# Performance work log

Hardware: AMD Instinct MI355X
Metric: run time of the kernel (lower is better)

## Reference

```python
import jax, jax.numpy as jnp
import numpy as np
from jax import lax

NMS_THRESH = 0.7
PRE_NMS_TOPK = 1000
POST_NMS_TOPK = 256
MIN_SIZE = 0.0


def setup_inputs() -> dict:
    key = jax.random.key(0)
    ks = jax.random.split(key, 4)
    N, C, Hf, Wf, P = 2, 128, 256, 256, 9
    x = jax.random.normal(ks[0], (N, C, Hf, Wf), jnp.float32)
    # small weight scales keep exp(offsets*stride) in a sane range (offsets head is zero-init in torch)
    W_conv = jax.random.normal(ks[1], (C, C, 3, 3), jnp.float32) * 0.05
    b_conv = jnp.zeros((C,), jnp.float32)
    W_off = jax.random.normal(ks[2], (2 * P, C), jnp.float32) * 0.01
    b_off = jnp.zeros((2 * P,), jnp.float32)
    W_log = jax.random.normal(ks[3], (1, C), jnp.float32) * 0.05
    b_log = jnp.zeros((1,), jnp.float32)
    return {"x": x, "W_conv": W_conv, "b_conv": b_conv, "W_off": W_off,
            "b_off": b_off, "W_log": W_log, "b_log": b_log,
            "image_h": 2048, "image_w": 2048}


def _forward_dense(x, W_conv, b_conv, W_off, b_off, W_log, b_log, image_h, image_w):
    N, C, Hf, Wf = x.shape
    t = lax.conv_general_dilated(x, W_conv, (1, 1), ((1, 1), (1, 1)),
                                 dimension_numbers=("NCHW", "OIHW", "NCHW"))
    t = jax.nn.relu(t + b_conv[None, :, None, None])
    logits = jnp.einsum("nchw,oc->nohw", t, W_log) + b_log[None, :, None, None]  # (N,1,Hf,Wf)
    off = jnp.einsum("nchw,oc->nohw", t, W_off) + b_off[None, :, None, None]      # (N,18,Hf,Wf)
    scale = image_w / Wf  # rescale() asserts scale_x == scale_y
    off = jnp.exp(off * scale) - 1.0
    # offsets2coordinates -- faithful to the torch code, including the H/W linspace
    # swap (ys spans image W over Hf points, xs spans image H over Wf points);
    # benign for square images.
    ys_lin = jnp.linspace(0.0, image_w - 1.0, Hf)
    xs_lin = jnp.linspace(0.0, image_h - 1.0, Wf)
    ys = jnp.broadcast_to(ys_lin[:, None], (Hf, Wf))
    xs = jnp.broadcast_to(xs_lin[None, :], (Hf, Wf))
    coords = off.reshape(N, 9, 2, Hf, Wf) + jnp.stack([xs, ys], 0)[None, None]
    cx = jnp.clip(coords[:, :, 0], 0.0, image_w - 1.0)  # clamp(0, W-1)
    cy = jnp.clip(coords[:, :, 1], 0.0, image_h - 1.0)  # clamp(0, H-1)
    # predict_proposals: min/max over the 9 points -> [N, Hf*Wf, 4]
    boxes = jnp.stack([cx.min(1), cy.min(1), cx.max(1), cy.max(1)], -1).reshape(N, Hf * Wf, 4)
    scores = logits.reshape(N, Hf * Wf)
    return scores, boxes


def _iou_matrix(b):
    x1, y1, x2, y2 = b[:, 0], b[:, 1], b[:, 2], b[:, 3]
    area = (x2 - x1) * (y2 - y1)
    iw = jnp.clip(jnp.minimum(x2[:, None], x2[None, :]) - jnp.maximum(x1[:, None], x1[None, :]), 0.0)
    ih = jnp.clip(jnp.minimum(y2[:, None], y2[None, :]) - jnp.maximum(y1[:, None], y1[None, :]), 0.0)
    inter = iw * ih
    return inter / (area[:, None] + area[None, :] - inter + 1e-9)


def _nms_one_image(scores, boxes):
    # pre-NMS topk (scores already returned sorted descending by top_k)
    sc, idx = lax.top_k(scores, PRE_NMS_TOPK)
    b = boxes[idx]
    w = b[:, 2] - b[:, 0]
    h = b[:, 3] - b[:, 1]
    valid = (w >= MIN_SIZE) & (h >= MIN_SIZE)
    sc = jnp.where(valid, sc, -jnp.inf)
    iou = _iou_matrix(b)
    ar = jnp.arange(PRE_NMS_TOPK)

    def body(i, sup):
        alive = (~sup[i]) & valid[i]
        return sup | ((iou[i] > NMS_THRESH) & (ar > i) & alive)

    sup = lax.fori_loop(0, PRE_NMS_TOPK, body, jnp.zeros((PRE_NMS_TOPK,), bool))
    keep_sc = jnp.where(sup, -jnp.inf, sc)
    final_sc, fidx = lax.top_k(keep_sc, POST_NMS_TOPK)
    return b[fidx], final_sc


def reference(x, W_conv, b_conv, W_off, b_off, W_log, b_log, image_h, image_w):
    scores, boxes = _forward_dense(x, W_conv, b_conv, W_off, b_off, W_log, b_log, image_h, image_w)
    out = jnp.concatenate([scores[..., None], boxes], axis=-1)  # (N, Hf*Wf, 5)
    kept_boxes, kept_scores = jax.vmap(_nms_one_image)(scores, boxes)
    return out, kept_boxes, kept_scores
```

## Files before the change

### kernel.cpp

```cpp
#include <hip/hip_runtime.h>
#include <stdint.h>

typedef unsigned int u32;
typedef unsigned long long u64;
typedef __attribute__((ext_vector_type(8))) short short8;
typedef __attribute__((ext_vector_type(16))) float f32x16;

#define DEVI __device__ __forceinline__

constexpr int PRE_K = 1000;
constexpr int CAP = 8192;

constexpr size_t WF_OFF    = 0;
constexpr size_t HIST_OFF  = 884736;
constexpr size_t CNT_OFF   = 917504;
constexpr size_t CUT_OFF   = 917568;
constexpr size_t CAND_OFF  = 917632;
constexpr size_t TB_OFF    = 1048704;
constexpr size_t SCS_OFF   = 1080704;
constexpr size_t MASK_OFF  = 1088768;
constexpr size_t SCARR_OFF = 1350912;
constexpr size_t WS_NEED   = 1875200;

constexpr size_t KB_OFF = 655360;
constexpr size_t KS_OFF = 657408;

DEVI u32 fkey(float f) {
  u32 u = __float_as_uint(f);
  return (u & 0x80000000u) ? ~u : (u | 0x80000000u);
}

DEVI u64 shfl64(u64 v, int src) {
  int lo = __shfl((int)(u32)v, src, 64);
  int hi = __shfl((int)(u32)(v >> 32), src, 64);
  return ((u64)(u32)hi << 32) | (u64)(u32)lo;
}

DEVI u32 rne16(u32 u) { return (u + 0x7FFFu + ((u >> 16) & 1u)) >> 16; }

__global__ void wsplitk(const float* __restrict__ wc, float* __restrict__ wf) {
  int j = blockIdx.x * 256 + threadIdx.x;
  if (j >= 18432) return;
  int co = j / 144;
  int koct = j % 144;
  short8 h8, m8, l8;
#pragma unroll
  for (int jj = 0; jj < 8; ++jj) {
    int kk = koct * 8 + jj;
    int tap = kk >> 7, ci = kk & 127;
    float v = wc[(co * 128 + ci) * 9 + tap];
    u32 u0 = __float_as_uint(v);
    u32 hb = rne16(u0);
    float r1 = v - __uint_as_float(hb << 16);
    u32 u1 = __float_as_uint(r1);
    u32 mb = rne16(u1);
    float r2 = r1 - __uint_as_float(mb << 16);
    u32 lb = rne16(__float_as_uint(r2));
    h8[jj] = (short)hb; m8[jj] = (short)mb; l8[jj] = (short)lb;
  }
  int slot = ((koct & 1) << 5) + (co & 31);
  int kg = koct >> 1;
  int cblk = co >> 5;
  char* base = (char*)wf;
  *(short8*)(base + ((size_t)((0 * 4 + cblk) * 72 + kg) * 64 + slot) * 16) = h8;
  *(short8*)(base + ((size_t)((1 * 4 + cblk) * 72 + kg) * 64 + slot) * 16) = m8;
  *(short8*)(base + ((size_t)((2 * 4 + cblk) * 72 + kg) * 64 + slot) * 16) = l8;
}

__global__ __launch_bounds__(256, 2) void convk(
    const float* __restrict__ x, const float* __restrict__ wf,
    const float* __restrict__ bconv,
    const float* __restrict__ woff, const float* __restrict__ boff,
    const float* __restrict__ wlog, const float* __restrict__ blog,
    const int* __restrict__ ihp, const int* __restrict__ iwp,
    float* __restrict__ out, u32* __restrict__ hist, float* __restrict__ scarr)
{
  __shared__ union {
    float halo[10][18][36];
    float tch[2][32][132];
  } sm;

  const int tid = threadIdx.x;
  const int l = tid & 63, wv = tid >> 6;
  const int mhalf = wv >> 1, nhalf = wv & 1;
  const int lm = l & 31, lg = l >> 5;
  const int bx = blockIdx.x, by = blockIdx.y, n = blockIdx.z;

  f32x16 acc[2][2];
#pragma unroll
  for (int mi = 0; mi < 2; ++mi)
#pragma unroll
    for (int ni = 0; ni < 2; ++ni)
#pragma unroll
      for (int q = 0; q < 16; ++q) acc[mi][ni][q] = 0.f;

#pragma unroll 1
  for (int cb = 0; cb < 4; ++cb) {
    __syncthreads();
    for (int e = tid; e < 5760; e += 256) {
      int ci = e / 180, rem = e % 180;
      int hh = rem / 18, ww = rem % 18;
      int gh = by * 8 + hh - 1, gw = bx * 16 + ww - 1;
      float v = 0.f;
      if ((unsigned)gh < 256u && (unsigned)gw < 256u)
        v = x[(((size_t)n * 128 + cb * 32 + ci) * 256 + gh) * 256 + gw];
      sm.halo[hh][ww][ci] = v;
    }
    __syncthreads();

#pragma unroll 1
    for (int tap = 0; tap < 9; ++tap) {
      int dy = tap / 3 - 1, dx = tap % 3 - 1;
      short8 Af[3][2][2];
#pragma unroll
      for (int mi = 0; mi < 2; ++mi) {
        int hh = mhalf * 4 + mi * 2 + (lm >> 4) + dy + 1;
        int ww = (lm & 15) + dx + 1;
#pragma unroll
        for (int ks = 0; ks < 2; ++ks) {
          const float* ap = &sm.halo[hh][ww][ks * 16 + lg * 8];
          float4 va = *(const float4*)ap;
          float4 vb = *(const float4*)(ap + 4);
          float fv[8] = {va.x, va.y, va.z, va.w, vb.x, vb.y, vb.z, vb.w};
          short8 ah, am, al;
#pragma unroll
          for (int jj = 0; jj < 8; ++jj) {
            u32 u0 = __float_as_uint(fv[jj]);
            u32 hb = rne16(u0);
            float r1 = fv[jj] - __uint_as_float(hb << 16);
            u32 u1 = __float_as_uint(r1);
            u32 mb = rne16(u1);
            float r2 = r1 - __uint_as_float(mb << 16);
            u32 lb = rne16(__float_as_uint(r2));
            ah[jj] = (short)hb; am[jj] = (short)mb; al[jj] = (short)lb;
          }
          Af[0][mi][ks] = ah; Af[1][mi][ks] = am; Af[2][mi][ks] = al;
        }
      }
      const char* wfb = (const char*)wf;
#pragma unroll
      for (int sb = 0; sb < 3; ++sb) {
        short8 Bf[2][2];
#pragma unroll
        for (int ni = 0; ni < 2; ++ni)
#pragma unroll
          for (int ks = 0; ks < 2; ++ks) {
            int fid = (sb * 4 + nhalf * 2 + ni) * 72 + tap * 8 + cb * 2 + ks;
            Bf[ni][ks] = *(const short8*)(wfb + ((size_t)fid * 64 + l) * 16);
          }
#pragma unroll
        for (int sa = 0; sa < 3 - sb; ++sa)
#pragma unroll
          for (int mi = 0; mi < 2; ++mi)
#pragma unroll
            for (int ni = 0; ni < 2; ++ni)
#pragma unroll
              for (int ks = 0; ks < 2; ++ks)
                acc[mi][ni] = __builtin_amdgcn_mfma_f32_32x32x16_bf16(
                    Af[sa][mi][ks], Bf[ni][ks], acc[mi][ni], 0, 0, 0);
      }
    }
  }

  __syncthreads();
  const int ihv = ihp[0], iwv = iwp[0];
  float bcv[2];
  bcv[0] = bconv[nhalf * 64 + lm];
  bcv[1] = bconv[nhalf * 64 + 32 + lm];
  const int cq = l >> 4;
  const int pxl = (nhalf << 4) + (l & 15);
  const float scale = (float)iwv / 256.0f;

#pragma unroll
  for (int r = 0; r < 2; ++r) {
    if (r) __syncthreads();
#pragma unroll
    for (int ni = 0; ni < 2; ++ni)
#pragma unroll
      for (int rg = 0; rg < 16; ++rg) {
        int row = (rg & 3) + ((rg >> 2) << 3) + ((l >> 5) << 2);
        sm.tch[mhalf][row][(nhalf << 6) + (ni << 5) + lm] =
            fmaxf(acc[r][ni][rg] + bcv[ni], 0.f);
      }
    __syncthreads();

    float tv[32];
#pragma unroll
    for (int i = 0; i < 8; ++i) {
      float4 t4 = *(const float4*)&sm.tch[mhalf][pxl][(cq << 5) + (i << 2)];
      tv[i * 4 + 0] = t4.x; tv[i * 4 + 1] = t4.y;
      tv[i * 4 + 2] = t4.z; tv[i * 4 + 3] = t4.w;
    }
    float s19[19];
#pragma unroll
    for (int o = 0; o < 19; ++o) {
      const float* wh = (o < 18) ? (woff + o * 128) : wlog;
      const float4* w4 = (const float4*)(wh + (cq << 5));
      float a0 = 0.f;
#pragma unroll
      for (int i = 0; i < 8; ++i) {
        float4 wv4 = w4[i];
        a0 = fmaf(tv[i * 4 + 0], wv4.x, a0);
        a0 = fmaf(tv[i * 4 + 1], wv4.y, a0);
        a0 = fmaf(tv[i * 4 + 2], wv4.z, a0);
        a0 = fmaf(tv[i * 4 + 3], wv4.w, a0);
      }
      s19[o] = a0;
    }
#pragma unroll
    for (int o = 0; o < 19; ++o) {
      s19[o] += __shfl_xor(s19[o], 16, 64);
      s19[o] += __shfl_xor(s19[o], 32, 64);
    }
    if (cq == 0) {
      int bpx = (mhalf << 6) + (r << 5) + pxl;
      int ph = bpx >> 4, pw = bpx & 15;
      int gh = by * 8 + ph, gw = bx * 16 + pw;
      float sc = s19[18] + blog[0];
      float xv = (float)((double)gw * ((double)(ihv - 1) / 255.0));
      float yv = (float)((double)gh * ((double)(iwv - 1) / 255.0));
      float mnx = __builtin_inff(), mny = __builtin_inff();
      float mxx = -__builtin_inff(), mxy = -__builtin_inff();
#pragma unroll
      for (int p = 0; p < 9; ++p) {
        float ox = expf((s19[2 * p] + boff[2 * p]) * scale) - 1.f + xv;
        float oy = expf((s19[2 * p + 1] + boff[2 * p + 1]) * scale) - 1.f + yv;
        float cx2 = fminf(fmaxf(ox, 0.f), (float)(iwv - 1));
        float cy2 = fminf(fmaxf(oy, 0.f), (float)(ihv - 1));
        mnx = fminf(mnx, cx2); mxx = fmaxf(mxx, cx2);
        mny = fminf(mny, cy2); mxy = fmaxf(mxy, cy2);
      }
      size_t pix = (size_t)n * 65536 + (size_t)gh * 256 + gw;
      float* rec = out + pix * 5;
      rec[0] = sc; rec[1] = mnx; rec[2] = mny; rec[3] = mxx; rec[4] = mxy;
      if (scarr) scarr[pix] = sc;
      atomicAdd(&hist[n * 4096 + (fkey(sc) >> 20)], 1u);
    }
  }
}

__global__ __launch_bounds__(256) void cutoffk(const u32* __restrict__ hist, u32* __restrict__ cut) {
  int n = blockIdx.x;
  const u32* h = hist + n * 4096;
  __shared__ u32 pre[256];
  int t = threadIdx.x;
  u32 s0 = 0;
  for (int k = 0; k < 16; ++k) s0 += h[4095 - (t * 16 + k)];
  pre[t] = s0;
  __syncthreads();
  for (int off = 1; off < 256; off <<= 1) {
    u32 add = (t >= off) ? pre[t - off] : 0u;
    __syncthreads();
    pre[t] += add;
    __syncthreads();
  }
  u32 incl = pre[t];
  u32 excl = incl - s0;
  if (incl >= (u32)PRE_K && excl < (u32)PRE_K) {
    u32 cum = excl;
    for (int k = 0; k < 16; ++k) {
      int b = 4095 - (t * 16 + k);
      cum += h[b];
      if (cum >= (u32)PRE_K) { cut[n] = ((u32)b) << 20; break; }
    }
  }
}

__global__ void collectk(const float* __restrict__ out, const float* __restrict__ scarr,
                         const u32* __restrict__ cut,
                         u32* __restrict__ cnt, u64* __restrict__ cand) {
  int e = blockIdx.x * 256 + threadIdx.x;
  int n = e >> 16;
  u32 pix = e & 65535;
  float sc = scarr ? scarr[e] : out[((size_t)n * 65536 + pix) * 5];
  u32 key = fkey(sc);
  if (key >= cut[n]) {
    u32 pos = atomicAdd(&cnt[n], 1u);
    if (pos < (u32)CAP)
      cand[(size_t)n * CAP + pos] = ((u64)key << 32) | (u64)(0xFFFFFFFFu - pix);
  }
}

__global__ __launch_bounds__(1024) void ranksel(const u64* __restrict__ cand, const u32* __restrict__ cnt,
                                                const float* __restrict__ out,
                                                float* __restrict__ tb, float* __restrict__ scs) {
  int n = blockIdx.x;
  int t = threadIdx.x;
  __shared__ u64 d[CAP];
  u32 m = cnt[n]; if (m > (u32)CAP) m = CAP;
  for (int i = t; i < (int)m; i += 1024) d[i] = cand[(size_t)n * CAP + i];
  __syncthreads();
  for (int i = t; i < (int)m; i += 1024) {
    u64 ki = d[i];
    u32 r = 0;
    for (u32 j = 0; j < m; ++j) r += (d[j] > ki) ? 1u : 0u;
    if (r < (u32)PRE_K) {
      u32 pix = 0xFFFFFFFFu - (u32)(ki & 0xFFFFFFFFull);
      const float* rec = out + ((size_t)n * 65536 + pix) * 5;
      float sc = rec[0];
      float b0 = rec[1], b1 = rec[2], b2 = rec[3], b3 = rec[4];
      bool valid = ((b2 - b0) >= 0.f) && ((b3 - b1) >= 0.f);
      scs[n * PRE_K + r] = valid ? sc : -__builtin_inff();
      float* tbp = tb + ((size_t)n * PRE_K + r) * 4;
      tbp[0] = b0; tbp[1] = b1; tbp[2] = b2; tbp[3] = b3;
    }
  }
}

__global__ __launch_bounds__(1024) void maskk(const float* __restrict__ tb, u64* __restrict__ maskw) {
  int c = blockIdx.x;
  int n = blockIdx.y;
  int t = threadIdx.x;
  __shared__ float bx[PRE_K][4];
  for (int e = t; e < PRE_K * 4; e += 1024) ((float*)bx)[e] = tb[(size_t)n * PRE_K * 4 + e];
  __syncthreads();
  u64 accm = 0;
  if (t < PRE_K) {
    float x1 = bx[t][0], y1 = bx[t][1], x2 = bx[t][2], y2 = bx[t][3];
    float ai = (x2 - x1) * (y2 - y1);
    int j0 = max(t + 1, c * 64), j1 = min(PRE_K, c * 64 + 64);
    for (int j = j0; j < j1; ++j) {
      float u1 = bx[j][0], v1 = bx[j][1], u2 = bx[j][2], v2 = bx[j][3];
      float aj = (u2 - u1) * (v2 - v1);
      float iw = fminf(x2, u2) - fmaxf(x1, u1); iw = fmaxf(iw, 0.f);
      float ih = fminf(y2, v2) - fmaxf(y1, v1); ih = fmaxf(ih, 0.f);
      float inter = iw * ih;
      float iou = inter / (ai + aj - inter + 1e-9f);
      if (iou > 0.7f) accm |= (1ull << (j & 63));
    }
  }
  maskw[((size_t)n * 1024 + t) * 16 + c] = accm;
}

__global__ __launch_bounds__(64) void finalk(const u64* __restrict__ maskw,
                                             const float* __restrict__ scs,
                                             const float* __restrict__ tb,
                                             float* __restrict__ out) {
  int n = blockIdx.x;
  int lane = threadIdx.x;
  __shared__ float lsc[1024];
  __shared__ unsigned short ordA[1024];
  __shared__ unsigned short ordB[1024];
  for (int e = lane; e < 1024; e += 64)
    lsc[e] = (e < PRE_K) ? scs[n * PRE_K + e] : -__builtin_inff();
  __syncthreads();

  u64 sup = 0;
#pragma unroll
  for (int c = 0; c < 16; ++c) {
    u64 b = __ballot(!(lsc[c * 64 + lane] > -__builtin_inff()));
    if (lane == c) sup = b;
  }

  const u64* gm = maskw + (size_t)n * 1024 * 16;
  u64 pre[16];
#pragma unroll
  for (int d = 0; d < 16; ++d)
    pre[d] = (lane < 16) ? gm[d * 16 + lane] : 0ull;

  for (int i0 = 0; i0 < 1024; i0 += 16) {
#pragma unroll
    for (int d = 0; d < 16; ++d) {
      int i = i0 + d;
      u64 mi = pre[d];
      int nx = i + 16;
      pre[d] = (nx < 1024 && lane < 16) ? gm[(size_t)nx * 16 + lane] : 0ull;
      int w = i >> 6;
      u64 sw = shfl64(sup, w);
      bool supbit = (sw >> (i & 63)) & 1ull;
      if (!supbit) sup |= mi;
    }
  }

  u64 ltm = (1ull << lane) - 1ull;
  u32 baseA = 0, baseB = 0;
  for (int c = 0; c < 16; ++c) {
    int i = c * 64 + lane;
    u64 sw = shfl64(sup, c);
    bool bit = (sw >> lane) & 1ull;
    bool vi = i < PRE_K;
    bool sf = vi && !bit && (lsc[vi ? i : 0] > -__builtin_inff());
    u64 mA = __ballot(sf);
    u64 mB = __ballot(vi && !sf);
    if (sf) ordA[baseA + __popcll(mA & ltm)] = (unsigned short)i;
    else if (vi) ordB[baseB + __popcll(mB & ltm)] = (unsigned short)i;
    baseA += (u32)__popcll(mA);
    baseB += (u32)__popcll(mB);
  }
  __syncthreads();

  for (int r = 0; r < 4; ++r) {
    int k = r * 64 + lane;
    int fi; float v;
    if (k < (int)baseA) { fi = ordA[k]; v = lsc[fi]; }
    else { fi = ordB[k - baseA]; v = -__builtin_inff(); }
    const float* bp = tb + ((size_t)n * PRE_K + fi) * 4;
    float* kb = out + KB_OFF + ((size_t)n * 256 + k) * 4;
    kb[0] = bp[0]; kb[1] = bp[1]; kb[2] = bp[2]; kb[3] = bp[3];
    out[KS_OFF + (size_t)n * 256 + k] = v;
  }
}

extern "C" void kernel_launch(void* const* d_in, const int* in_sizes, int n_in,
                              void* d_out, int out_size, void* d_ws, size_t ws_size,
                              hipStream_t stream) {
  const float* x     = (const float*)d_in[0];
  const float* wc    = (const float*)d_in[1];
  const float* bconv = (const float*)d_in[2];
  const float* woff  = (const float*)d_in[3];
  const float* boff  = (const float*)d_in[4];
  const float* wlog  = (const float*)d_in[5];
  const float* blog  = (const float*)d_in[6];
  const int* ihp     = (const int*)d_in[7];
  const int* iwp     = (const int*)d_in[8];
  float* out = (float*)d_out;
  char* ws = (char*)d_ws;

  float* wf   = (float*)(ws + WF_OFF);
  u32* hist   = (u32*)(ws + HIST_OFF);
  u32* cnt    = (u32*)(ws + CNT_OFF);
  u32* cut    = (u32*)(ws + CUT_OFF);
  u64* cand   = (u64*)(ws + CAND_OFF);
  float* tb   = (float*)(ws + TB_OFF);
  float* scs  = (float*)(ws + SCS_OFF);
  u64* maskw  = (u64*)(ws + MASK_OFF);
  float* scarr = (ws_size >= WS_NEED) ? (float*)(ws + SCARR_OFF) : nullptr;

  hipMemsetAsync(ws + HIST_OFF, 0, (CAND_OFF - HIST_OFF), stream);
  hipLaunchKernelGGL(wsplitk, dim3(72), dim3(256), 0, stream, wc, wf);
  hipLaunchKernelGGL(convk, dim3(16, 32, 2), dim3(256), 0, stream,
                     x, wf, bconv, woff, boff, wlog, blog, ihp, iwp, out, hist, scarr);
  hipLaunchKernelGGL(cutoffk, dim3(2), dim3(256), 0, stream, hist, cut);
  hipLaunchKernelGGL(collectk, dim3(512), dim3(256), 0, stream, out, scarr, cut, cnt, cand);
  hipLaunchKernelGGL(ranksel, dim3(2), dim3(1024), 0, stream, cand, cnt, out, tb, scs);
  hipLaunchKernelGGL(maskk, dim3(16, 2), dim3(1024), 0, stream, tb, maskw);
  hipLaunchKernelGGL(finalk, dim3(2), dim3(64), 0, stream, maskw, scs, tb, out);
}
```

Baseline: 629.9 us.

## Pre-split conv inputs into bf16 planes in LDS and fuse the NMS pipeline kernels

The conv kernel now splits each input value into three bf16 parts once, when it loads the halo, and keeps them as 16-bit planes in shared memory. This removes the per-tap re-splitting of the A fragments. Channel chunks shrink to 16, LDS use falls, and launch bounds are raised to 4 blocks per CU, with a serialized epilogue through a smaller staging buffer. The histogram cutoff is folded into the collect kernel, and rank selection, IoU mask and final NMS are merged into one kernel per image. The memset is moved into the weight-split kernel. The trade-offs are more barriers in the epilogue, and an IoU mask stage that now runs on only 2 blocks instead of 32, which adds serial work.

```diff
diff --git a/kernel.cpp b/kernel.cpp
--- a/kernel.cpp
+++ b/kernel.cpp
@@ -3,6 +3,7 @@
 
 typedef unsigned int u32;
 typedef unsigned long long u64;
+typedef __attribute__((ext_vector_type(4))) short short4v;
 typedef __attribute__((ext_vector_type(8))) short short8;
 typedef __attribute__((ext_vector_type(16))) float f32x16;
 
@@ -14,10 +15,7 @@
 constexpr size_t WF_OFF    = 0;
 constexpr size_t HIST_OFF  = 884736;
 constexpr size_t CNT_OFF   = 917504;
-constexpr size_t CUT_OFF   = 917568;
 constexpr size_t CAND_OFF  = 917632;
-constexpr size_t TB_OFF    = 1048704;
-constexpr size_t SCS_OFF   = 1080704;
 constexpr size_t MASK_OFF  = 1088768;
 constexpr size_t SCARR_OFF = 1350912;
 constexpr size_t WS_NEED   = 1875200;
@@ -38,8 +36,11 @@
 
 DEVI u32 rne16(u32 u) { return (u + 0x7FFFu + ((u >> 16) & 1u)) >> 16; }
 
-__global__ void wsplitk(const float* __restrict__ wc, float* __restrict__ wf) {
+__global__ void wsplitk(const float* __restrict__ wc, float* __restrict__ wf,
+                        u32* __restrict__ hist, u32* __restrict__ cnt) {
   int j = blockIdx.x * 256 + threadIdx.x;
+  if (j < 8192) hist[j] = 0;
+  if (j < 2) cnt[j] = 0;
   if (j >= 18432) return;
   int co = j / 144;
   int koct = j % 144;
@@ -52,8 +53,7 @@
     u32 u0 = __float_as_uint(v);
     u32 hb = rne16(u0);
     float r1 = v - __uint_as_float(hb << 16);
-    u32 u1 = __float_as_uint(r1);
-    u32 mb = rne16(u1);
+    u32 mb = rne16(__float_as_uint(r1));
     float r2 = r1 - __uint_as_float(mb << 16);
     u32 lb = rne16(__float_as_uint(r2));
     h8[jj] = (short)hb; m8[jj] = (short)mb; l8[jj] = (short)lb;
@@ -67,7 +67,7 @@
   *(short8*)(base + ((size_t)((2 * 4 + cblk) * 72 + kg) * 64 + slot) * 16) = l8;
 }
 
-__global__ __launch_bounds__(256, 2) void convk(
+__global__ __launch_bounds__(256, 4) void convk(
     const float* __restrict__ x, const float* __restrict__ wf,
     const float* __restrict__ bconv,
     const float* __restrict__ woff, const float* __restrict__ boff,
@@ -76,8 +76,8 @@
     float* __restrict__ out, u32* __restrict__ hist, float* __restrict__ scarr)
 {
   __shared__ union {
-    float halo[10][18][36];
-    float tch[2][32][132];
+    unsigned short pl[3 * 3600];
+    float tq[32][132];
   } sm;
 
   const int tid = threadIdx.x;
@@ -94,70 +94,65 @@
 #pragma unroll
       for (int q = 0; q < 16; ++q) acc[mi][ni][q] = 0.f;
 
+  const char* wfb = (const char*)wf;
+
 #pragma unroll 1
-  for (int cb = 0; cb < 4; ++cb) {
+  for (int cc = 0; cc < 8; ++cc) {
     __syncthreads();
-    for (int e = tid; e < 5760; e += 256) {
+    const float* xbase = x + ((size_t)n * 128 + cc * 16) * 65536;
+    for (int e = tid; e < 2880; e += 256) {
       int ci = e / 180, rem = e % 180;
       int hh = rem / 18, ww = rem % 18;
       int gh = by * 8 + hh - 1, gw = bx * 16 + ww - 1;
       float v = 0.f;
       if ((unsigned)gh < 256u && (unsigned)gw < 256u)
-        v = x[(((size_t)n * 128 + cb * 32 + ci) * 256 + gh) * 256 + gw];
-      sm.halo[hh][ww][ci] = v;
+        v = xbase[(size_t)ci * 65536 + gh * 256 + gw];
+      u32 u0 = __float_as_uint(v);
+      u32 hb = rne16(u0);
+      float r1 = v - __uint_as_float(hb << 16);
+      u32 mb = rne16(__float_as_uint(r1));
+      float r2 = r1 - __uint_as_float(mb << 16);
+      u32 lb = rne16(__float_as_uint(r2));
+      int idx = (hh * 18 + ww) * 20 + ci;
+      sm.pl[idx] = (unsigned short)hb;
+      sm.pl[idx + 3600] = (unsigned short)mb;
+      sm.pl[idx + 7200] = (unsigned short)lb;
     }
     __syncthreads();
 
 #pragma unroll 1
     for (int tap = 0; tap < 9; ++tap) {
       int dy = tap / 3 - 1, dx = tap % 3 - 1;
-      short8 Af[3][2][2];
+      short8 Af[3][2];
 #pragma unroll
       for (int mi = 0; mi < 2; ++mi) {
         int hh = mhalf * 4 + mi * 2 + (lm >> 4) + dy + 1;
         int ww = (lm & 15) + dx + 1;
-#pragma unroll
-        for (int ks = 0; ks < 2; ++ks) {
-          const float* ap = &sm.halo[hh][ww][ks * 16 + lg * 8];
-          float4 va = *(const float4*)ap;
-          float4 vb = *(const float4*)(ap + 4);
-          float fv[8] = {va.x, va.y, va.z, va.w, vb.x, vb.y, vb.z, vb.w};
-          short8 ah, am, al;
-#pragma unroll
-          for (int jj = 0; jj < 8; ++jj) {
-            u32 u0 = __float_as_uint(fv[jj]);
-            u32 hb = rne16(u0);
-            float r1 = fv[jj] - __uint_as_float(hb << 16);
-            u32 u1 = __float_as_uint(r1);
-            u32 mb = rne16(u1);
-            float r2 = r1 - __uint_as_float(mb << 16);
-            u32 lb = rne16(__float_as_uint(r2));
-            ah[jj] = (short)hb; am[jj] = (short)mb; al[jj] = (short)lb;
-          }
-          Af[0][mi][ks] = ah; Af[1][mi][ks] = am; Af[2][mi][ks] = al;
-        }
-      }
-      const char* wfb = (const char*)wf;
+        int base = (hh * 18 + ww) * 20 + lg * 8;
+#pragma unroll
+        for (int s = 0; s < 3; ++s) {
+          short4v a0 = *(const short4v*)&sm.pl[s * 3600 + base];
+          short4v a1 = *(const short4v*)&sm.pl[s * 3600 + base + 4];
+          short8 v8 = {a0[0], a0[1], a0[2], a0[3], a1[0], a1[1], a1[2], a1[3]};
+          Af[s][mi] = v8;
+        }
+      }
 #pragma unroll
       for (int sb = 0; sb < 3; ++sb) {
-        short8 Bf[2][2];
-#pragma unroll
-        for (int ni = 0; ni < 2; ++ni)
-#pragma unroll
-          for (int ks = 0; ks < 2; ++ks) {
-            int fid = (sb * 4 + nhalf * 2 + ni) * 72 + tap * 8 + cb * 2 + ks;
-            Bf[ni][ks] = *(const short8*)(wfb + ((size_t)fid * 64 + l) * 16);
-          }
+        short8 Bf[2];
+#pragma unroll
+        for (int ni = 0; ni < 2; ++ni) {
+          int fid = (sb * 4 + nhalf * 2 + ni) * 72 + tap * 8 + cc;
+          Bf[ni] = *(const short8*)(wfb + ((size_t)fid * 64 + l) * 16);
+        }
 #pragma unroll
         for (int sa = 0; sa < 3 - sb; ++sa)
 #pragma unroll
           for (int mi = 0; mi < 2; ++mi)
 #pragma unroll
             for (int ni = 0; ni < 2; ++ni)
-#pragma unroll
-              for (int ks = 0; ks < 2; ++ks)
-                acc[mi][ni] = __builtin_amdgcn_mfma_f32_32x32x16_bf16(
-                    Af[sa][mi][ks], Bf[ni][ks], acc[mi][ni], 0, 0, 0);
+              acc[mi][ni] = __builtin_amdgcn_mfma_f32_32x32x16_bf16(
+                  Af[sa][mi], Bf[ni], acc[mi][ni], 0, 0, 0);
       }
     }
   }
@@ -171,79 +166,90 @@
   const int pxl = (nhalf << 4) + (l & 15);
   const float scale = (float)iwv / 256.0f;
 
-#pragma unroll
-  for (int r = 0; r < 2; ++r) {
-    if (r) __syncthreads();
-#pragma unroll
-    for (int ni = 0; ni < 2; ++ni)
-#pragma unroll
-      for (int rg = 0; rg < 16; ++rg) {
-        int row = (rg & 3) + ((rg >> 2) << 3) + ((l >> 5) << 2);
-        sm.tch[mhalf][row][(nhalf << 6) + (ni << 5) + lm] =
-            fmaxf(acc[r][ni][rg] + bcv[ni], 0.f);
-      }
-    __syncthreads();
-
-    float tv[32];
-#pragma unroll
-    for (int i = 0; i < 8; ++i) {
-      float4 t4 = *(const float4*)&sm.tch[mhalf][pxl][(cq << 5) + (i << 2)];
-      tv[i * 4 + 0] = t4.x; tv[i * 4 + 1] = t4.y;
-      tv[i * 4 + 2] = t4.z; tv[i * 4 + 3] = t4.w;
-    }
-    float s19[19];
-#pragma unroll
-    for (int o = 0; o < 19; ++o) {
-      const float* wh = (o < 18) ? (woff + o * 128) : wlog;
-      const float4* w4 = (const float4*)(wh + (cq << 5));
-      float a0 = 0.f;
-#pragma unroll
-      for (int i = 0; i < 8; ++i) {
-        float4 wv4 = w4[i];
-        a0 = fmaf(tv[i * 4 + 0], wv4.x, a0);
-        a0 = fmaf(tv[i * 4 + 1], wv4.y, a0);
-        a0 = fmaf(tv[i * 4 + 2], wv4.z, a0);
-        a0 = fmaf(tv[i * 4 + 3], wv4.w, a0);
-      }
-      s19[o] = a0;
-    }
-#pragma unroll
-    for (int o = 0; o < 19; ++o) {
-      s19[o] += __shfl_xor(s19[o], 16, 64);
-      s19[o] += __shfl_xor(s19[o], 32, 64);
-    }
-    if (cq == 0) {
-      int bpx = (mhalf << 6) + (r << 5) + pxl;
-      int ph = bpx >> 4, pw = bpx & 15;
-      int gh = by * 8 + ph, gw = bx * 16 + pw;
-      float sc = s19[18] + blog[0];
-      float xv = (float)((double)gw * ((double)(ihv - 1) / 255.0));
-      float yv = (float)((double)gh * ((double)(iwv - 1) / 255.0));
-      float mnx = __builtin_inff(), mny = __builtin_inff();
-      float mxx = -__builtin_inff(), mxy = -__builtin_inff();
-#pragma unroll
-      for (int p = 0; p < 9; ++p) {
-        float ox = expf((s19[2 * p] + boff[2 * p]) * scale) - 1.f + xv;
-        float oy = expf((s19[2 * p + 1] + boff[2 * p + 1]) * scale) - 1.f + yv;
-        float cx2 = fminf(fmaxf(ox, 0.f), (float)(iwv - 1));
-        float cy2 = fminf(fmaxf(oy, 0.f), (float)(ihv - 1));
-        mnx = fminf(mnx, cx2); mxx = fmaxf(mxx, cx2);
-        mny = fminf(mny, cy2); mxy = fmaxf(mxy, cy2);
-      }
-      size_t pix = (size_t)n * 65536 + (size_t)gh * 256 + gw;
-      float* rec = out + pix * 5;
-      rec[0] = sc; rec[1] = mnx; rec[2] = mny; rec[3] = mxx; rec[4] = mxy;
-      if (scarr) scarr[pix] = sc;
-      atomicAdd(&hist[n * 4096 + (fkey(sc) >> 20)], 1u);
-    }
-  }
-}
-
-__global__ __launch_bounds__(256) void cutoffk(const u32* __restrict__ hist, u32* __restrict__ cut) {
-  int n = blockIdx.x;
+#pragma unroll 1
+  for (int mh = 0; mh < 2; ++mh) {
+#pragma unroll 1
+    for (int r = 0; r < 2; ++r) {
+      if (mh || r) __syncthreads();
+      if (mhalf == mh) {
+#pragma unroll
+        for (int ni = 0; ni < 2; ++ni)
+#pragma unroll
+          for (int rg = 0; rg < 16; ++rg) {
+            int row = (rg & 3) + ((rg >> 2) << 3) + ((l >> 5) << 2);
+            sm.tq[row][(nhalf << 6) + (ni << 5) + lm] =
+                fmaxf((r ? acc[1][ni][rg] : acc[0][ni][rg]) + bcv[ni], 0.f);
+          }
+      }
+      __syncthreads();
+      if (mhalf == mh) {
+        float tv[32];
+#pragma unroll
+        for (int i = 0; i < 8; ++i) {
+          float4 t4 = *(const float4*)&sm.tq[pxl][(cq << 5) + (i << 2)];
+          tv[i * 4 + 0] = t4.x; tv[i * 4 + 1] = t4.y;
+          tv[i * 4 + 2] = t4.z; tv[i * 4 + 3] = t4.w;
+        }
+        float s19[19];
+#pragma unroll
+        for (int o = 0; o < 19; ++o) {
+          const float* wh = (o < 18) ? (woff + o * 128) : wlog;
+          const float4* w4 = (const float4*)(wh + (cq << 5));
+          float a0 = 0.f;
+#pragma unroll
+          for (int i = 0; i < 8; ++i) {
+            float4 wv4 = w4[i];
+            a0 = fmaf(tv[i * 4 + 0], wv4.x, a0);
+            a0 = fmaf(tv[i * 4 + 1], wv4.y, a0);
+            a0 = fmaf(tv[i * 4 + 2], wv4.z, a0);
+            a0 = fmaf(tv[i * 4 + 3], wv4.w, a0);
+          }
+          s19[o] = a0;
+        }
+#pragma unroll
+        for (int o = 0; o < 19; ++o) {
+          s19[o] += __shfl_xor(s19[o], 16, 64);
+          s19[o] += __shfl_xor(s19[o], 32, 64);
+        }
+        if (cq == 0) {
+          int bpx = (mh << 6) + (r << 5) + pxl;
+          int ph = bpx >> 4, pw = bpx & 15;
+          int gh = by * 8 + ph, gw = bx * 16 + pw;
+          float sc = s19[18] + blog[0];
+          float xv = (float)((double)gw * ((double)(ihv - 1) / 255.0));
+          float yv = (float)((double)gh * ((double)(iwv - 1) / 255.0));
+          float mnx = __builtin_inff(), mny = __builtin_inff();
+          float mxx = -__builtin_inff(), mxy = -__builtin_inff();
+#pragma unroll
+          for (int p = 0; p < 9; ++p) {
+            float ox = expf((s19[2 * p] + boff[2 * p]) * scale) - 1.f + xv;
+            float oy = expf((s19[2 * p + 1] + boff[2 * p + 1]) * scale) - 1.f + yv;
+            float cx2 = fminf(fmaxf(ox, 0.f), (float)(iwv - 1));
+            float cy2 = fminf(fmaxf(oy, 0.f), (float)(ihv - 1));
+            mnx = fminf(mnx, cx2); mxx = fmaxf(mxx, cx2);
+            mny = fminf(mny, cy2); mxy = fmaxf(mxy, cy2);
+          }
+          size_t pix = (size_t)n * 65536 + (size_t)gh * 256 + gw;
+          float* rec = out + pix * 5;
+          rec[0] = sc; rec[1] = mnx; rec[2] = mny; rec[3] = mxx; rec[4] = mxy;
+          if (scarr) scarr[pix] = sc;
+          atomicAdd(&hist[n * 4096 + (fkey(sc) >> 20)], 1u);
+        }
+      }
+    }
+  }
+}
+
+__global__ __launch_bounds__(256) void collectk(const float* __restrict__ outr,
+                                                const float* __restrict__ scarr,
+                                                const u32* __restrict__ hist,
+                                                u32* __restrict__ cnt, u64* __restrict__ cand) {
+  int e = blockIdx.x * 256 + threadIdx.x;
+  int n = e >> 16;
+  int t = threadIdx.x;
+  __shared__ u32 pre[256];
+  __shared__ u32 cutv;
   const u32* h = hist + n * 4096;
-  __shared__ u32 pre[256];
-  int t = threadIdx.x;
   u32 s0 = 0;
   for (int k = 0; k < 16; ++k) s0 += h[4095 - (t * 16 + k)];
   pre[t] = s0;
@@ -254,150 +260,148 @@
     pre[t] += add;
     __syncthreads();
   }
-  u32 incl = pre[t];
-  u32 excl = incl - s0;
+  u32 incl = pre[t], excl = incl - s0;
   if (incl >= (u32)PRE_K && excl < (u32)PRE_K) {
     u32 cum = excl;
     for (int k = 0; k < 16; ++k) {
       int b = 4095 - (t * 16 + k);
       cum += h[b];
-      if (cum >= (u32)PRE_K) { cut[n] = ((u32)b) << 20; break; }
-    }
-  }
-}
-
-__global__ void collectk(const float* __restrict__ out, const float* __restrict__ scarr,
-                         const u32* __restrict__ cut,
-                         u32* __restrict__ cnt, u64* __restrict__ cand) {
-  int e = blockIdx.x * 256 + threadIdx.x;
-  int n = e >> 16;
+      if (cum >= (u32)PRE_K) { cutv = ((u32)b) << 20; break; }
+    }
+  }
+  __syncthreads();
+  u32 cut = cutv;
   u32 pix = e & 65535;
-  float sc = scarr ? scarr[e] : out[((size_t)n * 65536 + pix) * 5];
+  float sc = scarr ? scarr[e] : outr[((size_t)n * 65536 + pix) * 5];
   u32 key = fkey(sc);
-  if (key >= cut[n]) {
+  if (key >= cut) {
     u32 pos = atomicAdd(&cnt[n], 1u);
     if (pos < (u32)CAP)
       cand[(size_t)n * CAP + pos] = ((u64)key << 32) | (u64)(0xFFFFFFFFu - pix);
   }
 }
 
-__global__ __launch_bounds__(1024) void ranksel(const u64* __restrict__ cand, const u32* __restrict__ cnt,
-                                                const float* __restrict__ out,
-                                                float* __restrict__ tb, float* __restrict__ scs) {
+__global__ __launch_bounds__(1024) void rmfk(const u64* __restrict__ cand,
+                                             const u32* __restrict__ cnt,
+                                             const float* __restrict__ outr,
+                                             u64* __restrict__ maskw,
+                                             float* __restrict__ out) {
   int n = blockIdx.x;
   int t = threadIdx.x;
-  __shared__ u64 d[CAP];
+  struct Sel {
+    float bx[PRE_K][4];
+    float lsc[1024];
+    unsigned short ordA[1024];
+    unsigned short ordB[1024];
+  };
+  __shared__ union { u64 d[CAP]; Sel s; } u;
+
   u32 m = cnt[n]; if (m > (u32)CAP) m = CAP;
-  for (int i = t; i < (int)m; i += 1024) d[i] = cand[(size_t)n * CAP + i];
-  __syncthreads();
+  for (int i = t; i < (int)m; i += 1024) u.d[i] = cand[(size_t)n * CAP + i];
+  __syncthreads();
+  int rr[8]; u32 rpix[8]; int nri = 0;
   for (int i = t; i < (int)m; i += 1024) {
-    u64 ki = d[i];
+    u64 ki = u.d[i];
     u32 r = 0;
-    for (u32 j = 0; j < m; ++j) r += (d[j] > ki) ? 1u : 0u;
+    for (u32 j = 0; j < m; ++j) r += (u.d[j] > ki) ? 1u : 0u;
     if (r < (u32)PRE_K) {
-      u32 pix = 0xFFFFFFFFu - (u32)(ki & 0xFFFFFFFFull);
-      const float* rec = out + ((size_t)n * 65536 + pix) * 5;
-      float sc = rec[0];
-      float b0 = rec[1], b1 = rec[2], b2 = rec[3], b3 = rec[4];
-      bool valid = ((b2 - b0) >= 0.f) && ((b3 - b1) >= 0.f);
-      scs[n * PRE_K + r] = valid ? sc : -__builtin_inff();
-      float* tbp = tb + ((size_t)n * PRE_K + r) * 4;
-      tbp[0] = b0; tbp[1] = b1; tbp[2] = b2; tbp[3] = b3;
-    }
-  }
-}
-
-__global__ __launch_bounds__(1024) void maskk(const float* __restrict__ tb, u64* __restrict__ maskw) {
-  int c = blockIdx.x;
-  int n = blockIdx.y;
-  int t = threadIdx.x;
-  __shared__ float bx[PRE_K][4];
-  for (int e = t; e < PRE_K * 4; e += 1024) ((float*)bx)[e] = tb[(size_t)n * PRE_K * 4 + e];
-  __syncthreads();
-  u64 accm = 0;
-  if (t < PRE_K) {
-    float x1 = bx[t][0], y1 = bx[t][1], x2 = bx[t][2], y2 = bx[t][3];
-    float ai = (x2 - x1) * (y2 - y1);
-    int j0 = max(t + 1, c * 64), j1 = min(PRE_K, c * 64 + 64);
-    for (int j = j0; j < j1; ++j) {
-      float u1 = bx[j][0], v1 = bx[j][1], u2 = bx[j][2], v2 = bx[j][3];
-      float aj = (u2 - u1) * (v2 - v1);
-      float iw = fminf(x2, u2) - fmaxf(x1, u1); iw = fmaxf(iw, 0.f);
-      float ih = fminf(y2, v2) - fmaxf(y1, v1); ih = fmaxf(ih, 0.f);
-      float inter = iw * ih;
-      float iou = inter / (ai + aj - inter + 1e-9f);
-      if (iou > 0.7f) accm |= (1ull << (j & 63));
-    }
-  }
-  maskw[((size_t)n * 1024 + t) * 16 + c] = accm;
-}
-
-__global__ __launch_bounds__(64) void finalk(const u64* __restrict__ maskw,
-                                             const float* __restrict__ scs,
-                                             const float* __restrict__ tb,
-                                             float* __restrict__ out) {
-  int n = blockIdx.x;
-  int lane = threadIdx.x;
-  __shared__ float lsc[1024];
-  __shared__ unsigned short ordA[1024];
-  __shared__ unsigned short ordB[1024];
-  for (int e = lane; e < 1024; e += 64)
-    lsc[e] = (e < PRE_K) ? scs[n * PRE_K + e] : -__builtin_inff();
-  __syncthreads();
-
-  u64 sup = 0;
-#pragma unroll
-  for (int c = 0; c < 16; ++c) {
-    u64 b = __ballot(!(lsc[c * 64 + lane] > -__builtin_inff()));
-    if (lane == c) sup = b;
-  }
-
-  const u64* gm = maskw + (size_t)n * 1024 * 16;
-  u64 pre[16];
-#pragma unroll
-  for (int d = 0; d < 16; ++d)
-    pre[d] = (lane < 16) ? gm[d * 16 + lane] : 0ull;
-
-  for (int i0 = 0; i0 < 1024; i0 += 16) {
-#pragma unroll
-    for (int d = 0; d < 16; ++d) {
-      int i = i0 + d;
-      u64 mi = pre[d];
-      int nx = i + 16;
-      pre[d] = (nx < 1024 && lane < 16) ? gm[(size_t)nx * 16 + lane] : 0ull;
-      int w = i >> 6;
-      u64 sw = shfl64(sup, w);
-      bool supbit = (sw >> (i & 63)) & 1ull;
-      if (!supbit) sup |= mi;
-    }
-  }
-
-  u64 ltm = (1ull << lane) - 1ull;
-  u32 baseA = 0, baseB = 0;
-  for (int c = 0; c < 16; ++c) {
-    int i = c * 64 + lane;
-    u64 sw = shfl64(sup, c);
-    bool bit = (sw >> lane) & 1ull;
-    bool vi = i < PRE_K;
-    bool sf = vi && !bit && (lsc[vi ? i : 0] > -__builtin_inff());
-    u64 mA = __ballot(sf);
-    u64 mB = __ballot(vi && !sf);
-    if (sf) ordA[baseA + __popcll(mA & ltm)] = (unsigned short)i;
-    else if (vi) ordB[baseB + __popcll(mB & ltm)] = (unsigned short)i;
-    baseA += (u32)__popcll(mA);
-    baseB += (u32)__popcll(mB);
-  }
-  __syncthreads();
-
-  for (int r = 0; r < 4; ++r) {
-    int k = r * 64 + lane;
-    int fi; float v;
-    if (k < (int)baseA) { fi = ordA[k]; v = lsc[fi]; }
-    else { fi = ordB[k - baseA]; v = -__builtin_inff(); }
-    const float* bp = tb + ((size_t)n * PRE_K + fi) * 4;
-    float* kb = out + KB_OFF + ((size_t)n * 256 + k) * 4;
-    kb[0] = bp[0]; kb[1] = bp[1]; kb[2] = bp[2]; kb[3] = bp[3];
-    out[KS_OFF + (size_t)n * 256 + k] = v;
+      rr[nri] = (int)r;
+      rpix[nri] = 0xFFFFFFFFu - (u32)(ki & 0xFFFFFFFFull);
+      ++nri;
+    }
+  }
+  __syncthreads();
+  u.s.lsc[t] = -__builtin_inff();
+  __syncthreads();
+  for (int q = 0; q < nri; ++q) {
+    int r = rr[q]; u32 pix = rpix[q];
+    const float* rec = outr + ((size_t)n * 65536 + pix) * 5;
+    float sc = rec[0];
+    float b0 = rec[1], b1 = rec[2], b2 = rec[3], b3 = rec[4];
+    bool valid = ((b2 - b0) >= 0.f) && ((b3 - b1) >= 0.f);
+    u.s.lsc[r] = valid ? sc : -__builtin_inff();
+    u.s.bx[r][0] = b0; u.s.bx[r][1] = b1; u.s.bx[r][2] = b2; u.s.bx[r][3] = b3;
+  }
+  __syncthreads();
+  {
+    float x1 = 0.f, y1 = 0.f, x2 = 0.f, y2 = 0.f, ai = 0.f;
+    if (t < PRE_K) {
+      x1 = u.s.bx[t][0]; y1 = u.s.bx[t][1]; x2 = u.s.bx[t][2]; y2 = u.s.bx[t][3];
+      ai = (x2 - x1) * (y2 - y1);
+    }
+    for (int w = 0; w < 16; ++w) {
+      u64 accm = 0;
+      if (t < PRE_K) {
+        int j0 = max(t + 1, w * 64), j1 = min(PRE_K, w * 64 + 64);
+        for (int j = j0; j < j1; ++j) {
+          float u1 = u.s.bx[j][0], v1 = u.s.bx[j][1], u2 = u.s.bx[j][2], v2 = u.s.bx[j][3];
+          float aj = (u2 - u1) * (v2 - v1);
+          float iw = fminf(x2, u2) - fmaxf(x1, u1); iw = fmaxf(iw, 0.f);
+          float ih = fminf(y2, v2) - fmaxf(y1, v1); ih = fmaxf(ih, 0.f);
+          float inter = iw * ih;
+          float iou = inter / (ai + aj - inter + 1e-9f);
+          if (iou > 0.7f) accm |= (1ull << (j & 63));
+        }
+      }
+      maskw[((size_t)n * 1024 + t) * 16 + w] = accm;
+    }
+  }
+  __threadfence();
+  __syncthreads();
+  if (t < 64) {
+    int lane = t;
+    u64 sup = 0;
+#pragma unroll
+    for (int c = 0; c < 16; ++c) {
+      u64 b = __ballot(!(u.s.lsc[c * 64 + lane] > -__builtin_inff()));
+      if (lane == c) sup = b;
+    }
+    const u64* gm = maskw + (size_t)n * 1024 * 16;
+    u64 pre16[16];
+#pragma unroll
+    for (int d = 0; d < 16; ++d)
+      pre16[d] = (lane < 16) ? gm[d * 16 + lane] : 0ull;
+
+    for (int i0 = 0; i0 < 1024; i0 += 16) {
+#pragma unroll
+      for (int d = 0; d < 16; ++d) {
+        int i = i0 + d;
+        u64 mi = pre16[d];
+        int nx = i + 16;
+        pre16[d] = (nx < 1024 && lane < 16) ? gm[(size_t)nx * 16 + lane] : 0ull;
+        int w = i >> 6;
+        u64 sw = shfl64(sup, w);
+        bool supbit = (sw >> (i & 63)) & 1ull;
+        if (!supbit) sup |= mi;
+      }
+    }
+
+    u64 ltm = (1ull << lane) - 1ull;
+    u32 baseA = 0, baseB = 0;
+    for (int c = 0; c < 16; ++c) {
+      int i = c * 64 + lane;
+      u64 sw = shfl64(sup, c);
+      bool bit = (sw >> lane) & 1ull;
+      bool vi = i < PRE_K;
+      bool sf = vi && !bit && (u.s.lsc[vi ? i : 0] > -__builtin_inff());
+      u64 mA = __ballot(sf);
+      u64 mB = __ballot(vi && !sf);
+      if (sf) u.s.ordA[baseA + __popcll(mA & ltm)] = (unsigned short)i;
+      else if (vi) u.s.ordB[baseB + __popcll(mB & ltm)] = (unsigned short)i;
+      baseA += (u32)__popcll(mA);
+      baseB += (u32)__popcll(mB);
+    }
+
+    for (int r = 0; r < 4; ++r) {
+      int k = r * 64 + lane;
+      int fi; float v;
+      if (k < (int)baseA) { fi = u.s.ordA[k]; v = u.s.lsc[fi]; }
+      else { fi = u.s.ordB[k - baseA]; v = -__builtin_inff(); }
+      float* kb = out + KB_OFF + ((size_t)n * 256 + k) * 4;
+      kb[0] = u.s.bx[fi][0]; kb[1] = u.s.bx[fi][1];
+      kb[2] = u.s.bx[fi][2]; kb[3] = u.s.bx[fi][3];
+      out[KS_OFF + (size_t)n * 256 + k] = v;
+    }
   }
 }
 
@@ -416,23 +420,16 @@
   float* out = (float*)d_out;
   char* ws = (char*)d_ws;
 
-  float* wf   = (float*)(ws + WF_OFF);
-  u32* hist   = (u32*)(ws + HIST_OFF);
-  u32* cnt    = (u32*)(ws + CNT_OFF);
-  u32* cut    = (u32*)(ws + CUT_OFF);
-  u64* cand   = (u64*)(ws + CAND_OFF);
-  float* tb   = (float*)(ws + TB_OFF);
-  float* scs  = (float*)(ws + SCS_OFF);
-  u64* maskw  = (u64*)(ws + MASK_OFF);
+  float* wf    = (float*)(ws + WF_OFF);
+  u32* hist    = (u32*)(ws + HIST_OFF);
+  u32* cnt     = (u32*)(ws + CNT_OFF);
+  u64* cand    = (u64*)(ws + CAND_OFF);
+  u64* maskw   = (u64*)(ws + MASK_OFF);
   float* scarr = (ws_size >= WS_NEED) ? (float*)(ws + SCARR_OFF) : nullptr;
 
-  hipMemsetAsync(ws + HIST_OFF, 0, (CAND_OFF - HIST_OFF), stream);
-  hipLaunchKernelGGL(wsplitk, dim3(72), dim3(256), 0, stream, wc, wf);
+  hipLaunchKernelGGL(wsplitk, dim3(72), dim3(256), 0, stream, wc, wf, hist, cnt);
   hipLaunchKernelGGL(convk, dim3(16, 32, 2), dim3(256), 0, stream,
                      x, wf, bconv, woff, boff, wlog, blog, ihp, iwp, out, hist, scarr);
-  hipLaunchKernelGGL(cutoffk, dim3(2), dim3(256), 0, stream, hist, cut);
-  hipLaunchKernelGGL(collectk, dim3(512), dim3(256), 0, stream, out, scarr, cut, cnt, cand);
-  hipLaunchKernelGGL(ranksel, dim3(2), dim3(1024), 0, stream, cand, cnt, out, tb, scs);
-  hipLaunchKernelGGL(maskk, dim3(16, 2), dim3(1024), 0, stream, tb, maskw);
-  hipLaunchKernelGGL(finalk, dim3(2), dim3(64), 0, stream, maskw, scs, tb, out);
-}
+  hipLaunchKernelGGL(collectk, dim3(512), dim3(256), 0, stream, out, scarr, hist, cnt, cand);
+  hipLaunchKernelGGL(rmfk, dim3(2), dim3(1024), 0, stream, cand, cnt, out, maskw, out);
+}
```

Result: slower. 711.0 us (+12.9%).
